# Optimization experiments

Measured on AMD Instinct MI355X. Metric: run time of the kernel, lower is better.

## Reference

```python
import jax, jax.numpy as jnp
import numpy as np

EMBED_DIM = 64
CODEBOOK_SIZE = 2048
COMMITMENT_COST = 1.0


def setup_inputs() -> dict:
    key = jax.random.key(0)
    k1, k2 = jax.random.split(key)
    inputs = jax.random.normal(k1, (32, 2048, EMBED_DIM), dtype=jnp.float32)
    embeddings = jax.random.normal(k2, (EMBED_DIM, CODEBOOK_SIZE), dtype=jnp.float32)
    return {"inputs": inputs, "embeddings": embeddings}


def reference(inputs, embeddings):
    # inference path (training=False): deterministic argmin quantization.
    D = embeddings.shape[0]
    K = embeddings.shape[1]
    flat = inputs.reshape(-1, D)                       # [N, D]
    similarity = flat @ embeddings                     # [N, K]
    distances = (jnp.sum(flat * flat, axis=1, keepdims=True)
                 - 2.0 * similarity
                 + jnp.sum(embeddings * embeddings, axis=0, keepdims=True))
    # gumbel layer with temperature 0 / eval mode -> argmax(-dist) == argmin(dist)
    flat_indices = jnp.argmax(-distances, axis=1)      # [N]
    encodings = jax.nn.one_hot(flat_indices, K, dtype=jnp.float32)  # [N, K]
    encoding_indices = flat_indices.reshape(inputs.shape[:-1])      # [B, T]
    quantized = jnp.take(embeddings.T, encoding_indices, axis=0)    # [B, T, D]
    e_latent_loss = jnp.mean(jnp.square(jax.lax.stop_gradient(quantized) - inputs))
    loss = e_latent_loss * COMMITMENT_COST
    return quantized, encodings, encoding_indices, loss
```

## Files before the change

kernel.cpp:

```cpp
#include <hip/hip_runtime.h>

#define N_ROWS 65536
#define DDIM   64
#define KCODES 2048
#define NB     128
#define CHUNK  256
#define NCHUNK (KCODES / CHUNK)
#define TAU    0.05f

#define Q_OFF    ((size_t)0)
#define ENC_OFF  ((size_t)N_ROWS * DDIM)
#define IDX_OFF  (ENC_OFF + (size_t)N_ROWS * KCODES)
#define LOSS_OFF (IDX_OFF + (size_t)N_ROWS)
#define INV_ND (1.0f / ((float)N_ROWS * (float)DDIM))

#define WS_ESQ_OFF   (524288)
#define WS_FLAGS_OFF (532480)

typedef __attribute__((ext_vector_type(8))) short short8;
typedef __attribute__((ext_vector_type(4))) float f32x4;

__device__ __forceinline__ unsigned short f2bf(float f) {
    unsigned u = __float_as_uint(f);
    u += 0x7FFFu + ((u >> 16) & 1u);
    return (unsigned short)(u >> 16);
}
__device__ __forceinline__ float bf2f(unsigned short h) {
    return __uint_as_float(((unsigned)h) << 16);
}

__global__ void vq_prep(const float* __restrict__ emb, char* __restrict__ ws,
                        float* __restrict__ out) {
    int t = blockIdx.x * 256 + threadIdx.x;
    int code = t & (KCODES - 1);
    int d    = t >> 11;
    float v = emb[(size_t)d * KCODES + code];
    unsigned short hi = f2bf(v);
    unsigned short lo = f2bf(v - bf2f(hi));
    int ch = code >> 8;
    int lc = code & 255;
    int kk = d ^ ((code & 7) << 3);
    short* base = (short*)ws + (size_t)ch * 32768 + lc * 64 + kk;
    base[0]     = (short)hi;
    base[16384] = (short)lo;
    if (t < KCODES) {
        float s = 0.f;
        for (int dd = 0; dd < DDIM; ++dd) {
            float e = emb[(size_t)dd * KCODES + t];
            s += e * e;
        }
        ((float*)(ws + WS_ESQ_OFF))[t] = s;
    }
    if (t == 0) out[LOSS_OFF] = 0.f;
}

__launch_bounds__(256, 2)
__global__ void vq_main(const float* __restrict__ x, const float* __restrict__ emb,
                        const char* __restrict__ ws, int* __restrict__ flags,
                        float* __restrict__ out) {
    __shared__ __align__(16) short Bs[32768];
    const int tid = threadIdx.x;
    const int l = tid & 63, w = tid >> 6;
    const int q = l >> 4, c = l & 15;
    const int r0 = blockIdx.x * NB;
    const float* esq = (const float*)(ws + WS_ESQ_OFF);

    short8 ah0[2], ah1[2], al0[2], al1[2];
    #pragma unroll
    for (int rt = 0; rt < 2; ++rt) {
        int row = r0 + w * 32 + rt * 16 + c;
        const float4* xr = (const float4*)(x + (size_t)row * DDIM);
        float4 f0 = xr[q * 2],     f1 = xr[q * 2 + 1];
        float4 f2 = xr[8 + q * 2], f3 = xr[8 + q * 2 + 1];
        float a0[8] = {f0.x,f0.y,f0.z,f0.w,f1.x,f1.y,f1.z,f1.w};
        float a1[8] = {f2.x,f2.y,f2.z,f2.w,f3.x,f3.y,f3.z,f3.w};
        #pragma unroll
        for (int j = 0; j < 8; ++j) {
            unsigned short h0 = f2bf(a0[j]);
            ah0[rt][j] = (short)h0;
            al0[rt][j] = (short)f2bf(a0[j] - bf2f(h0));
            unsigned short h1 = f2bf(a1[j]);
            ah1[rt][j] = (short)h1;
            al1[rt][j] = (short)f2bf(a1[j] - bf2f(h1));
        }
    }

    float m1[8], m2[8]; int i1[8];
    #pragma unroll
    for (int s = 0; s < 8; ++s) { m1[s] = 3.4e38f; m2[s] = 3.4e38f; i1[s] = 0; }

    for (int ch = 0; ch < NCHUNK; ++ch) {
        const int kc = ch * CHUNK;
        __syncthreads();
        {
            const int4* g4 = (const int4*)(ws + (size_t)ch * 65536);
            int4* s4 = (int4*)Bs;
            #pragma unroll
            for (int i = 0; i < 16; ++i) s4[i * 256 + tid] = g4[i * 256 + tid];
        }
        __syncthreads();

        {
            float4 z = make_float4(0.f, 0.f, 0.f, 0.f);
            float* ebase = out + ENC_OFF + (size_t)r0 * KCODES + kc;
            #pragma unroll
            for (int j = 0; j < 32; ++j) {
                int s   = j * 256 + tid;
                int row = s >> 6;
                int c4  = s & 63;
                *(float4*)(ebase + (size_t)row * KCODES + (c4 << 2)) = z;
            }
        }

        const int swz = (c & 7) << 3;
        for (int t = 0; t < 16; ++t) {
            int codeL = t * 16 + c;
            const short* ph = Bs + codeL * 64;
            const short* pl = ph + 16384;
            int k0 = (q * 8) ^ swz;
            int k1 = (32 + q * 8) ^ swz;
            short8 bh0 = *(const short8*)(ph + k0);
            short8 bh1 = *(const short8*)(ph + k1);
            short8 bl0 = *(const short8*)(pl + k0);
            short8 bl1 = *(const short8*)(pl + k1);
            int   kidx = kc + t * 16 + c;
            float eq   = esq[kidx];
            #pragma unroll
            for (int rt = 0; rt < 2; ++rt) {
                f32x4 acc = {0.f, 0.f, 0.f, 0.f};
                acc = __builtin_amdgcn_mfma_f32_16x16x32_bf16(ah0[rt], bh0, acc, 0, 0, 0);
                acc = __builtin_amdgcn_mfma_f32_16x16x32_bf16(ah1[rt], bh1, acc, 0, 0, 0);
                acc = __builtin_amdgcn_mfma_f32_16x16x32_bf16(ah0[rt], bl0, acc, 0, 0, 0);
                acc = __builtin_amdgcn_mfma_f32_16x16x32_bf16(ah1[rt], bl1, acc, 0, 0, 0);
                acc = __builtin_amdgcn_mfma_f32_16x16x32_bf16(al0[rt], bh0, acc, 0, 0, 0);
                acc = __builtin_amdgcn_mfma_f32_16x16x32_bf16(al1[rt], bh1, acc, 0, 0, 0);
                #pragma unroll
                for (int g = 0; g < 4; ++g) {
                    float dist = fmaf(-2.f, acc[g], eq);
                    int s = rt * 4 + g;
                    bool better = dist < m1[s];
                    m2[s] = fminf(m2[s], fmaxf(m1[s], dist));
                    m1[s] = fminf(m1[s], dist);
                    i1[s] = better ? kidx : i1[s];
                }
            }
        }
    }

    __syncthreads();
    float* red  = (float*)Bs;
    int*   indS = (int*)(red + 6144);
    float* lred = red + 6144 + 128;

    #pragma unroll
    for (int rt = 0; rt < 2; ++rt)
        #pragma unroll
        for (int g = 0; g < 4; ++g) {
            int lrow = w * 32 + rt * 16 + q * 4 + g;
            float* p = red + (size_t)(lrow * 16 + c) * 3;
            p[0] = m1[rt * 4 + g];
            p[1] = (float)i1[rt * 4 + g];
            p[2] = m2[rt * 4 + g];
        }
    __syncthreads();

    if (tid < NB) {
        int row = tid;
        const float* p = red + (size_t)row * 48;
        float gm1 = 3.4e38f; int gi1 = 0x7fffffff; int wt = -1;
        for (int t = 0; t < 16; ++t) {
            float v  = p[t * 3 + 0];
            int   iv = (int)p[t * 3 + 1];
            if (v < gm1 || (v == gm1 && iv < gi1)) { gm1 = v; gi1 = iv; wt = t; }
        }
        float gm2 = 3.4e38f;
        for (int t = 0; t < 16; ++t) {
            float cand = (t == wt) ? p[t * 3 + 2] : p[t * 3 + 0];
            gm2 = fminf(gm2, cand);
        }
        int gr = r0 + row;
        out[IDX_OFF + gr] = (float)gi1;
        flags[gr] = (gm2 - gm1 < TAU) ? 1 : 0;
        indS[row] = gi1;
        out[ENC_OFF + (size_t)gr * KCODES + gi1] = 1.0f;
    }
    __syncthreads();

    float lpart = 0.f;
    for (int i = tid; i < NB * (DDIM / 4); i += 256) {
        int row = i >> 4;
        int d4  = (i & 15) << 2;
        int idx = indS[row];
        int gr  = r0 + row;
        float4 qv;
        qv.x = emb[(size_t)(d4 + 0) * KCODES + idx];
        qv.y = emb[(size_t)(d4 + 1) * KCODES + idx];
        qv.z = emb[(size_t)(d4 + 2) * KCODES + idx];
        qv.w = emb[(size_t)(d4 + 3) * KCODES + idx];
        *(float4*)(out + Q_OFF + (size_t)gr * DDIM + d4) = qv;
        float4 xv = *(const float4*)(x + (size_t)gr * DDIM + d4);
        float dx = qv.x - xv.x, dy = qv.y - xv.y, dz = qv.z - xv.z, dw = qv.w - xv.w;
        lpart += dx * dx + dy * dy + dz * dz + dw * dw;
    }
    #pragma unroll
    for (int o = 32; o > 0; o >>= 1) lpart += __shfl_down(lpart, o);
    if ((tid & 63) == 0) lred[tid >> 6] = lpart;
    __syncthreads();
    if (tid == 0)
        atomicAdd(out + LOSS_OFF, (lred[0] + lred[1] + lred[2] + lred[3]) * INV_ND);
}

__global__ void vq_refine(const float* __restrict__ x, const float* __restrict__ emb,
                          const int* __restrict__ flags, float* __restrict__ out) {
    const int lane = threadIdx.x & 63;
    const int wid  = threadIdx.x >> 6;
    for (int rr = 0; rr < 8; ++rr) {
        int row = (blockIdx.x * 4 + wid) * 8 + rr;
        if (flags[row] == 0) continue;
        const float* xr = x + (size_t)row * DDIM;
        double best = 1e300; int bidx = 0x7fffffff;
        for (int k = lane; k < KCODES; k += 64) {
            double s = 0.0, ee = 0.0;
            for (int d = 0; d < DDIM; ++d) {
                double e = (double)emb[(size_t)d * KCODES + k];
                s  = fma((double)xr[d], e, s);
                ee = fma(e, e, ee);
            }
            double dist = ee - 2.0 * s;
            if (dist < best) { best = dist; bidx = k; }
        }
        #pragma unroll
        for (int o = 32; o > 0; o >>= 1) {
            double ob = __shfl_down(best, o);
            int    oi = __shfl_down(bidx, o);
            if (ob < best || (ob == best && oi < bidx)) { best = ob; bidx = oi; }
        }
        bidx = __shfl(bidx, 0);
        int oldIdx = (int)out[IDX_OFF + row];
        if (bidx == oldIdx) continue;
        if (lane == 0) {
            out[IDX_OFF + row] = (float)bidx;
            out[ENC_OFF + (size_t)row * KCODES + oldIdx] = 0.f;
            out[ENC_OFF + (size_t)row * KCODES + bidx]   = 1.f;
        }
        float eN = emb[(size_t)lane * KCODES + bidx];
        float eO = emb[(size_t)lane * KCODES + oldIdx];
        float xv = xr[lane];
        out[Q_OFF + (size_t)row * DDIM + lane] = eN;
        float dn = eN - xv, dod = eO - xv;
        float delta = dn * dn - dod * dod;
        #pragma unroll
        for (int o = 32; o > 0; o >>= 1) delta += __shfl_down(delta, o);
        if (lane == 0) atomicAdd(out + LOSS_OFF, delta * INV_ND);
    }
}

extern "C" void kernel_launch(void* const* d_in, const int* in_sizes, int n_in,
                              void* d_out, int out_size, void* d_ws, size_t ws_size,
                              hipStream_t stream) {
    const float* x   = (const float*)d_in[0];
    const float* emb = (const float*)d_in[1];
    float* out   = (float*)d_out;
    char*  ws    = (char*)d_ws;
    int*   flags = (int*)(ws + WS_FLAGS_OFF);
    hipLaunchKernelGGL(vq_prep,   dim3(512),         dim3(256), 0, stream, emb, ws, out);
    hipLaunchKernelGGL(vq_main,   dim3(N_ROWS / NB), dim3(256), 0, stream, x, emb, ws, flags, out);
    hipLaunchKernelGGL(vq_refine, dim3(N_ROWS / 32), dim3(256), 0, stream, x, emb, flags, out);
}
```

Measured before the change: 759.2 us.

## Split argmin compute from one-hot, quantized and loss writes into separate kernel

The main kernel no longer zero-fills the 512 MB encodings buffer inside its MFMA chunk loop. It now only computes the argmin index and the refinement flag. A new vq_write kernel reads the stored indices and, in one pass, writes the dense one-hot rows, gathers the quantized vectors and accumulates the loss. This is meant to stop the huge store stream from competing with the distance computation and to avoid writing each winning slot twice. The cost is an extra kernel launch and a small reload of the indices from global memory.

```diff
diff --git a/kernel.cpp b/kernel.cpp
--- a/kernel.cpp
+++ b/kernel.cpp
@@ -55,15 +55,15 @@
 }
 
 __launch_bounds__(256, 2)
-__global__ void vq_main(const float* __restrict__ x, const float* __restrict__ emb,
-                        const char* __restrict__ ws, int* __restrict__ flags,
-                        float* __restrict__ out) {
+__global__ void vq_argmin(const float* __restrict__ x, const char* __restrict__ ws,
+                          float* __restrict__ out) {
     __shared__ __align__(16) short Bs[32768];
     const int tid = threadIdx.x;
     const int l = tid & 63, w = tid >> 6;
     const int q = l >> 4, c = l & 15;
     const int r0 = blockIdx.x * NB;
     const float* esq = (const float*)(ws + WS_ESQ_OFF);
+    int*   flags = (int*)(ws + WS_FLAGS_OFF);
 
     short8 ah0[2], ah1[2], al0[2], al1[2];
     #pragma unroll
@@ -99,18 +99,6 @@
             for (int i = 0; i < 16; ++i) s4[i * 256 + tid] = g4[i * 256 + tid];
         }
         __syncthreads();
-
-        {
-            float4 z = make_float4(0.f, 0.f, 0.f, 0.f);
-            float* ebase = out + ENC_OFF + (size_t)r0 * KCODES + kc;
-            #pragma unroll
-            for (int j = 0; j < 32; ++j) {
-                int s   = j * 256 + tid;
-                int row = s >> 6;
-                int c4  = s & 63;
-                *(float4*)(ebase + (size_t)row * KCODES + (c4 << 2)) = z;
-            }
-        }
 
         const int swz = (c & 7) << 3;
         for (int t = 0; t < 16; ++t) {
@@ -148,9 +136,7 @@
     }
 
     __syncthreads();
-    float* red  = (float*)Bs;
-    int*   indS = (int*)(red + 6144);
-    float* lred = red + 6144 + 128;
+    float* red = (float*)Bs;
 
     #pragma unroll
     for (int rt = 0; rt < 2; ++rt)
@@ -181,27 +167,52 @@
         int gr = r0 + row;
         out[IDX_OFF + gr] = (float)gi1;
         flags[gr] = (gm2 - gm1 < TAU) ? 1 : 0;
-        indS[row] = gi1;
-        out[ENC_OFF + (size_t)gr * KCODES + gi1] = 1.0f;
-    }
-    __syncthreads();
-
-    float lpart = 0.f;
-    for (int i = tid; i < NB * (DDIM / 4); i += 256) {
-        int row = i >> 4;
-        int d4  = (i & 15) << 2;
-        int idx = indS[row];
-        int gr  = r0 + row;
-        float4 qv;
-        qv.x = emb[(size_t)(d4 + 0) * KCODES + idx];
-        qv.y = emb[(size_t)(d4 + 1) * KCODES + idx];
-        qv.z = emb[(size_t)(d4 + 2) * KCODES + idx];
-        qv.w = emb[(size_t)(d4 + 3) * KCODES + idx];
-        *(float4*)(out + Q_OFF + (size_t)gr * DDIM + d4) = qv;
-        float4 xv = *(const float4*)(x + (size_t)gr * DDIM + d4);
-        float dx = qv.x - xv.x, dy = qv.y - xv.y, dz = qv.z - xv.z, dw = qv.w - xv.w;
-        lpart += dx * dx + dy * dy + dz * dz + dw * dw;
-    }
+    }
+}
+
+__global__ void vq_write(const float* __restrict__ x, const float* __restrict__ emb,
+                         float* __restrict__ out) {
+    const int tid  = threadIdx.x;
+    const int row0 = blockIdx.x * 16;
+    __shared__ float lred[4];
+    __shared__ int   idxS[16];
+
+    if (tid < 16) idxS[tid] = (int)out[IDX_OFF + row0 + tid];
+    __syncthreads();
+
+    int r  = tid >> 4;
+    int d4 = (tid & 15) << 2;
+    int rowq = row0 + r;
+    int idxq = idxS[r];
+    float4 qv;
+    qv.x = emb[(size_t)(d4 + 0) * KCODES + idxq];
+    qv.y = emb[(size_t)(d4 + 1) * KCODES + idxq];
+    qv.z = emb[(size_t)(d4 + 2) * KCODES + idxq];
+    qv.w = emb[(size_t)(d4 + 3) * KCODES + idxq];
+    *(float4*)(out + Q_OFF + (size_t)rowq * DDIM + d4) = qv;
+    float4 xv = *(const float4*)(x + (size_t)rowq * DDIM + d4);
+    float dx = qv.x - xv.x, dy = qv.y - xv.y, dz = qv.z - xv.z, dw = qv.w - xv.w;
+    float lpart = dx * dx + dy * dy + dz * dz + dw * dw;
+
+    const int base = tid << 3;
+    #pragma unroll 4
+    for (int rr = 0; rr < 16; ++rr) {
+        int row = row0 + rr;
+        int idx = idxS[rr];
+        float4 v0, v1;
+        v0.x = (base + 0 == idx) ? 1.f : 0.f;
+        v0.y = (base + 1 == idx) ? 1.f : 0.f;
+        v0.z = (base + 2 == idx) ? 1.f : 0.f;
+        v0.w = (base + 3 == idx) ? 1.f : 0.f;
+        v1.x = (base + 4 == idx) ? 1.f : 0.f;
+        v1.y = (base + 5 == idx) ? 1.f : 0.f;
+        v1.z = (base + 6 == idx) ? 1.f : 0.f;
+        v1.w = (base + 7 == idx) ? 1.f : 0.f;
+        float* p = out + ENC_OFF + (size_t)row * KCODES + base;
+        *(float4*)p       = v0;
+        *(float4*)(p + 4) = v1;
+    }
+
     #pragma unroll
     for (int o = 32; o > 0; o >>= 1) lpart += __shfl_down(lpart, o);
     if ((tid & 63) == 0) lred[tid >> 6] = lpart;
@@ -263,7 +274,8 @@
     float* out   = (float*)d_out;
     char*  ws    = (char*)d_ws;
     int*   flags = (int*)(ws + WS_FLAGS_OFF);
-    hipLaunchKernelGGL(vq_prep,   dim3(512),         dim3(256), 0, stream, emb, ws, out);
-    hipLaunchKernelGGL(vq_main,   dim3(N_ROWS / NB), dim3(256), 0, stream, x, emb, ws, flags, out);
-    hipLaunchKernelGGL(vq_refine, dim3(N_ROWS / 32), dim3(256), 0, stream, x, emb, flags, out);
-}
+    hipLaunchKernelGGL(vq_prep,   dim3(512),          dim3(256), 0, stream, emb, ws, out);
+    hipLaunchKernelGGL(vq_argmin, dim3(N_ROWS / NB),  dim3(256), 0, stream, x, ws, out);
+    hipLaunchKernelGGL(vq_write,  dim3(N_ROWS / 16),  dim3(256), 0, stream, x, emb, out);
+    hipLaunchKernelGGL(vq_refine, dim3(N_ROWS / 32),  dim3(256), 0, stream, x, emb, flags, out);
+}
```

Measured after the change: 1.005 ms. 32.4% more time.

## Split argmin and output writes into separate kernels with direct one-hot stores

Applied to the files above, without the earlier changes.

The fused main kernel is split into a compute-only argmin kernel and a separate write kernel. The argmin kernel no longer zero-fills the encodings inside its chunk loop. The write kernel reads the stored indices back and writes the one-hot rows in a single pass of coalesced float4 stores, then produces the quantized outputs and the loss. This removes the zero-then-scatter double write and frees the MFMA loop from store traffic. In exchange it adds a kernel launch, re-reads x and the indices, and gives up any overlap between the encoding stores and the distance computation.

```diff
diff --git a/kernel.cpp b/kernel.cpp
--- a/kernel.cpp
+++ b/kernel.cpp
@@ -55,15 +55,15 @@
 }
 
 __launch_bounds__(256, 2)
-__global__ void vq_main(const float* __restrict__ x, const float* __restrict__ emb,
-                        const char* __restrict__ ws, int* __restrict__ flags,
-                        float* __restrict__ out) {
+__global__ void vq_argmin(const float* __restrict__ x, const char* __restrict__ ws,
+                          float* __restrict__ out) {
     __shared__ __align__(16) short Bs[32768];
     const int tid = threadIdx.x;
     const int l = tid & 63, w = tid >> 6;
     const int q = l >> 4, c = l & 15;
     const int r0 = blockIdx.x * NB;
     const float* esq = (const float*)(ws + WS_ESQ_OFF);
+    int*   flags = (int*)(ws + WS_FLAGS_OFF);
 
     short8 ah0[2], ah1[2], al0[2], al1[2];
     #pragma unroll
@@ -99,18 +99,6 @@
             for (int i = 0; i < 16; ++i) s4[i * 256 + tid] = g4[i * 256 + tid];
         }
         __syncthreads();
-
-        {
-            float4 z = make_float4(0.f, 0.f, 0.f, 0.f);
-            float* ebase = out + ENC_OFF + (size_t)r0 * KCODES + kc;
-            #pragma unroll
-            for (int j = 0; j < 32; ++j) {
-                int s   = j * 256 + tid;
-                int row = s >> 6;
-                int c4  = s & 63;
-                *(float4*)(ebase + (size_t)row * KCODES + (c4 << 2)) = z;
-            }
-        }
 
         const int swz = (c & 7) << 3;
         for (int t = 0; t < 16; ++t) {
@@ -148,9 +136,7 @@
     }
 
     __syncthreads();
-    float* red  = (float*)Bs;
-    int*   indS = (int*)(red + 6144);
-    float* lred = red + 6144 + 128;
+    float* red = (float*)Bs;
 
     #pragma unroll
     for (int rt = 0; rt < 2; ++rt)
@@ -181,17 +167,26 @@
         int gr = r0 + row;
         out[IDX_OFF + gr] = (float)gi1;
         flags[gr] = (gm2 - gm1 < TAU) ? 1 : 0;
-        indS[row] = gi1;
-        out[ENC_OFF + (size_t)gr * KCODES + gi1] = 1.0f;
-    }
+    }
+}
+
+__launch_bounds__(256, 2)
+__global__ void vq_write(const float* __restrict__ x, const float* __restrict__ emb,
+                         float* __restrict__ out) {
+    const int tid  = threadIdx.x;
+    const int row0 = blockIdx.x * 128;
+    __shared__ float lred[4];
+    __shared__ int   idxS[128];
+
+    if (tid < 128) idxS[tid] = (int)out[IDX_OFF + row0 + tid];
     __syncthreads();
 
     float lpart = 0.f;
-    for (int i = tid; i < NB * (DDIM / 4); i += 256) {
+    for (int i = tid; i < 128 * 16; i += 256) {
         int row = i >> 4;
         int d4  = (i & 15) << 2;
-        int idx = indS[row];
-        int gr  = r0 + row;
+        int idx = idxS[row];
+        int gr  = row0 + row;
         float4 qv;
         qv.x = emb[(size_t)(d4 + 0) * KCODES + idx];
         qv.y = emb[(size_t)(d4 + 1) * KCODES + idx];
@@ -202,6 +197,26 @@
         float dx = qv.x - xv.x, dy = qv.y - xv.y, dz = qv.z - xv.z, dw = qv.w - xv.w;
         lpart += dx * dx + dy * dy + dz * dz + dw * dw;
     }
+
+    const int b0 = tid << 2;
+    const int b1 = (tid + 256) << 2;
+    #pragma unroll 4
+    for (int rr = 0; rr < 128; ++rr) {
+        int idx = idxS[rr];
+        float* p = out + ENC_OFF + (size_t)(row0 + rr) * KCODES;
+        float4 v0, v1;
+        v0.x = (b0 + 0 == idx) ? 1.f : 0.f;
+        v0.y = (b0 + 1 == idx) ? 1.f : 0.f;
+        v0.z = (b0 + 2 == idx) ? 1.f : 0.f;
+        v0.w = (b0 + 3 == idx) ? 1.f : 0.f;
+        v1.x = (b1 + 0 == idx) ? 1.f : 0.f;
+        v1.y = (b1 + 1 == idx) ? 1.f : 0.f;
+        v1.z = (b1 + 2 == idx) ? 1.f : 0.f;
+        v1.w = (b1 + 3 == idx) ? 1.f : 0.f;
+        *(float4*)(p + b0) = v0;
+        *(float4*)(p + b1) = v1;
+    }
+
     #pragma unroll
     for (int o = 32; o > 0; o >>= 1) lpart += __shfl_down(lpart, o);
     if ((tid & 63) == 0) lred[tid >> 6] = lpart;
@@ -263,7 +278,8 @@
     float* out   = (float*)d_out;
     char*  ws    = (char*)d_ws;
     int*   flags = (int*)(ws + WS_FLAGS_OFF);
-    hipLaunchKernelGGL(vq_prep,   dim3(512),         dim3(256), 0, stream, emb, ws, out);
-    hipLaunchKernelGGL(vq_main,   dim3(N_ROWS / NB), dim3(256), 0, stream, x, emb, ws, flags, out);
-    hipLaunchKernelGGL(vq_refine, dim3(N_ROWS / 32), dim3(256), 0, stream, x, emb, flags, out);
-}
+    hipLaunchKernelGGL(vq_prep,   dim3(512),          dim3(256), 0, stream, emb, ws, out);
+    hipLaunchKernelGGL(vq_argmin, dim3(N_ROWS / NB),  dim3(256), 0, stream, x, ws, out);
+    hipLaunchKernelGGL(vq_write,  dim3(N_ROWS / 128), dim3(256), 0, stream, x, emb, out);
+    hipLaunchKernelGGL(vq_refine, dim3(N_ROWS / 32),  dim3(256), 0, stream, x, emb, flags, out);
+}
```

Measured after the change: 876.4 us. 15.4% more time.
